# Performance work log

Measured on AMD Instinct MI355X. Metric: run time of the kernel, lower is better.

## Reference

```python
import math
import jax, jax.numpy as jnp
import numpy as np

B, L, C, H = 8, 1024, 1024, 16
D = C // H  # head_dim = 64
MAX_SCALE_MUL = math.log(100.0)


def setup_inputs() -> dict:
    key = jax.random.key(0)
    ks = jax.random.split(key, 8)
    x = jax.random.normal(ks[0], (B, L, C), dtype=jnp.float32)
    # rotary frequencies: angle(l, j) = l * theta^(-2j/D), stored as (cos, sin)
    theta = 10000.0
    inv_freq = theta ** (-jnp.arange(0, D, 2, dtype=jnp.float32) / D)  # [D/2]
    ang = jnp.arange(L, dtype=jnp.float32)[:, None] * inv_freq[None, :]  # [L, D/2]
    freqs_cis = jnp.stack([jnp.cos(ang), jnp.sin(ang)], axis=-1)  # [L, D/2, 2]
    attn_bias = jnp.zeros((1, 1, L, L), dtype=jnp.float32)
    W_qkv = jax.random.normal(ks[1], (3 * C, C), dtype=jnp.float32) * (1.0 / math.sqrt(C))
    q_bias = jnp.zeros((C,), dtype=jnp.float32)
    v_bias = jnp.zeros((C,), dtype=jnp.float32)
    scale_mul_log = jnp.full((1, H, 1, 1), math.log(4.0), dtype=jnp.float32)
    W_proj = jax.random.normal(ks[2], (C, C), dtype=jnp.float32) * (1.0 / math.sqrt(C))
    b_proj = jnp.zeros((C,), dtype=jnp.float32)
    return {"x": x, "freqs_cis": freqs_cis, "attn_bias": attn_bias,
            "W_qkv": W_qkv, "q_bias": q_bias, "v_bias": v_bias,
            "scale_mul_log": scale_mul_log, "W_proj": W_proj, "b_proj": b_proj}


def _l2norm(t):
    # F.normalize(t, dim=-1): t / max(||t||_2, eps)
    n = jnp.sqrt(jnp.sum(t * t, axis=-1, keepdims=True))
    return t / jnp.maximum(n, 1e-12)


def _rope(t, fr):
    # t: [B,H,L,D]; fr: [L,D/2,2] (cos,sin). Complex mul on adjacent pairs.
    b, h, l, d = t.shape
    t2 = t.reshape(b, h, l, d // 2, 2)
    c = fr[None, None, :, :, 0]
    s = fr[None, None, :, :, 1]
    re = t2[..., 0] * c - t2[..., 1] * s
    im = t2[..., 0] * s + t2[..., 1] * c
    return jnp.stack([re, im], axis=-1).reshape(b, h, l, d)


def reference(x, freqs_cis, attn_bias, W_qkv, q_bias, v_bias, scale_mul_log, W_proj, b_proj):
    b, l, c = x.shape
    bias = jnp.concatenate([q_bias, jnp.zeros_like(q_bias), v_bias])  # [3C]
    qkv = (x @ W_qkv.T + bias).reshape(b, l, 3, H, D)
    # permute(2,0,3,1,4) -> q,k,v each [B,H,L,D]
    q = jnp.transpose(qkv[:, :, 0], (0, 2, 1, 3))
    k = jnp.transpose(qkv[:, :, 1], (0, 2, 1, 3))
    v = jnp.transpose(qkv[:, :, 2], (0, 2, 1, 3))
    # attn_l2_norm path: learned per-head scale, softmax scale = 1
    scale_mul = jnp.exp(jnp.minimum(scale_mul_log, MAX_SCALE_MUL))  # [1,H,1,1]
    q = _l2norm(q) * scale_mul
    k = _l2norm(k)
    q = _rope(q, freqs_cis)
    k = _rope(k, freqs_cis)
    scores = jnp.einsum('bhqd,bhkd->bhqk', q, k) * 1.0 + attn_bias
    attn = jax.nn.softmax(scores, axis=-1)
    out = jnp.einsum('bhqk,bhkd->bhqd', attn, v)
    out = jnp.transpose(out, (0, 2, 1, 3)).reshape(b, l, c)
    return out @ W_proj.T + b_proj
```

## Files before the change

### kernel.cpp

```cpp
#include <hip/hip_runtime.h>
#include <math.h>

#define PB 8
#define PL 1024
#define PC 1024
#define PH 16
#define PD 64
#define MAX_SCALE_MUL 4.605170185988092f
#define LOG2E 1.4426950408889634f

typedef __attribute__((ext_vector_type(8))) short s16x8;
typedef __attribute__((ext_vector_type(4))) float f32x4;

#define MFMA16(a, b, c) __builtin_amdgcn_mfma_f32_16x16x32_bf16(a, b, c, 0, 0, 0)

#if __has_builtin(__builtin_amdgcn_exp2f)
#define EXP2(x) __builtin_amdgcn_exp2f(x)
#else
#define EXP2(x) exp2f(x)
#endif

__device__ __forceinline__ unsigned short f2bf(float f) {
    unsigned u = __float_as_uint(f);
    unsigned r = (u + 0x7fffu + ((u >> 16) & 1u)) >> 16;
    return (unsigned short)r;
}

__device__ __forceinline__ unsigned pk2bf(float a, float b) {
#if __has_builtin(__builtin_amdgcn_cvt_pk_bf16_f32)
    typedef __attribute__((ext_vector_type(2))) __bf16 bf16x2_t;
    bf16x2_t r = __builtin_amdgcn_cvt_pk_bf16_f32(a, b);
    return __builtin_bit_cast(unsigned, r);
#else
    return (unsigned)f2bf(a) | ((unsigned)f2bf(b) << 16);
#endif
}

__device__ __forceinline__ void gl2lds16(const void* g, void* l) {
    __builtin_amdgcn_global_load_lds(
        (const __attribute__((address_space(1))) unsigned int*)g,
        (__attribute__((address_space(3))) unsigned int*)l, 16, 0, 0);
}

__global__ __launch_bounds__(256) void bias_flag_kernel(
    const float* __restrict__ bias, int* __restrict__ flag)
{
    int idx = blockIdx.x * 256 + threadIdx.x;
    const float4* b4 = (const float4*)bias;
    bool nz = false;
#pragma unroll
    for (int i = 0; i < 4; i++) {
        float4 v = b4[idx * 4 + i];
        nz |= (v.x != 0.f) | (v.y != 0.f) | (v.z != 0.f) | (v.w != 0.f);
    }
    if (nz) atomicOr(flag, 1);
}

__global__ __launch_bounds__(256) void cast3_kernel(
    const float* __restrict__ a, const float* __restrict__ b,
    const float* __restrict__ c,
    unsigned short* __restrict__ oa, unsigned short* __restrict__ ob,
    unsigned short* __restrict__ oc)
{
    int blk = blockIdx.x;
    const float* src; unsigned short* dst; int base;
    if (blk < 8192)       { src = a; dst = oa; base = blk; }
    else if (blk < 11264) { src = b; dst = ob; base = blk - 8192; }
    else                  { src = c; dst = oc; base = blk - 11264; }
    int i = base * 256 + threadIdx.x;
    float4 v = ((const float4*)src)[i];
    ((uint2*)dst)[i] = make_uint2(pk2bf(v.x, v.y), pk2bf(v.z, v.w));
}

__global__ __launch_bounds__(256) void gemm_qkv_lean(
    const unsigned short* __restrict__ Xh,
    const unsigned short* __restrict__ Wh,
    const float* __restrict__ qb, const float* __restrict__ vb,
    unsigned short* __restrict__ Qh, unsigned short* __restrict__ Kh,
    unsigned short* __restrict__ Vh)
{
    __shared__ unsigned short As[128 * 32];
    __shared__ unsigned short Bs[128 * 32];
    const int tid  = threadIdx.x;
    const int wave = tid >> 6, lane = tid & 63;
    const int wm = wave & 1, wn = wave >> 1;
    const int quad = lane >> 4, rr = lane & 15;
    const int m0 = blockIdx.x * 128, n0 = blockIdx.y * 128;

    f32x4 acc[4][4];
#pragma unroll
    for (int i = 0; i < 4; i++)
#pragma unroll
        for (int j = 0; j < 4; j++) acc[i][j] = (f32x4){0.f, 0.f, 0.f, 0.f};

    const int rw = lane >> 2;
    const int cc = lane & 3;
    const int g  = cc ^ ((rw >> 1) & 3);
    const int srow = wave * 32 + rw;
    const unsigned short* gA0 = Xh + (size_t)(m0 + srow) * 1024 + g * 8;
    const unsigned short* gA1 = gA0 + (size_t)16 * 1024;
    const unsigned short* gB0 = Wh + (size_t)(n0 + srow) * 1024 + g * 8;
    const unsigned short* gB1 = gB0 + (size_t)16 * 1024;
    unsigned short* lA0 = &As[(wave * 32) * 32];
    unsigned short* lA1 = &As[(wave * 32 + 16) * 32];
    unsigned short* lB0 = &Bs[(wave * 32) * 32];
    unsigned short* lB1 = &Bs[(wave * 32 + 16) * 32];

    const int swz = (rr >> 1) & 3;
    const int coff = ((quad ^ swz) * 8);

    for (int k0 = 0; k0 < 1024; k0 += 32) {
        gl2lds16(gA0, lA0); gl2lds16(gA1, lA1);
        gl2lds16(gB0, lB0); gl2lds16(gB1, lB1);
        gA0 += 32; gA1 += 32; gB0 += 32; gB1 += 32;
        __syncthreads();

        s16x8 af[4], bf[4];
#pragma unroll
        for (int i = 0; i < 4; i++)
            af[i] = *(const s16x8*)&As[(wm * 64 + i * 16 + rr) * 32 + coff];
#pragma unroll
        for (int j = 0; j < 4; j++)
            bf[j] = *(const s16x8*)&Bs[(wn * 64 + j * 16 + rr) * 32 + coff];
#pragma unroll
        for (int i = 0; i < 4; i++)
#pragma unroll
            for (int j = 0; j < 4; j++)
                acc[i][j] = MFMA16(af[i], bf[j], acc[i][j]);
        __syncthreads();
    }

    const int b     = m0 >> 10;
    const int which = n0 >> 10;
    const int h     = ((n0 & 1023) + wn * 64) >> 6;
    const int lb0   = (m0 & 1023) + wm * 64;
    unsigned short* dst = (which == 0) ? Qh : ((which == 1) ? Kh : Vh);
    unsigned short* base = dst + ((size_t)(b * PH + h) * PL) * PD;

#pragma unroll
    for (int j = 0; j < 4; j++) {
        const int d = j * 16 + rr;
        float bias = 0.f;
        if (which == 0) bias = qb[h * 64 + d];
        if (which == 2) bias = vb[h * 64 + d];
#pragma unroll
        for (int i = 0; i < 4; i++) {
            const int l = lb0 + i * 16 + quad * 4;
#pragma unroll
            for (int reg = 0; reg < 4; reg++)
                base[(size_t)(l + reg) * PD + d] = f2bf(acc[i][j][reg] + bias);
        }
    }
}

__global__ __launch_bounds__(256) void postproc_kernel(
    unsigned short* __restrict__ Qh, unsigned short* __restrict__ Kh,
    const unsigned short* __restrict__ Vh, unsigned short* __restrict__ Vt,
    const float* __restrict__ freqs, const float* __restrict__ sml)
{
    const int blk = blockIdx.x;
    const int tid = threadIdx.x;

    if (blk < 32768) {
        const bool isQ = blk < 16384;
        const int rb = isQ ? blk : blk - 16384;
        const int row = rb * 8 + (tid >> 5);
        const int li  = tid & 31;
        const int h = (row >> 10) & (PH - 1);
        const int l = row & (PL - 1);

        unsigned short* buf = isQ ? Qh : Kh;
        unsigned* p = (unsigned*)(buf + (size_t)row * PD) + li;
        unsigned v = *p;
        float v0 = __uint_as_float(v << 16);
        float v1 = __uint_as_float(v & 0xffff0000u);

        float ss = fmaf(v0, v0, v1 * v1);
#pragma unroll
        for (int off = 1; off <= 16; off <<= 1) ss += __shfl_xor(ss, off);

        float smul = isQ ? (__expf(fminf(sml[h], MAX_SCALE_MUL)) * LOG2E) : 1.0f;
        float scale = smul / fmaxf(sqrtf(ss), 1e-12f);
        v0 *= scale; v1 *= scale;

        float2 cs = ((const float2*)freqs)[l * 32 + li];
        float re = v0 * cs.x - v1 * cs.y;
        float im = fmaf(v0, cs.y, v1 * cs.x);
        *p = pk2bf(re, im);
        return;
    }

    const int vblk = blk - 32768;
    const int bh = vblk >> 4;
    const int l0 = (vblk & 15) * 64;
#pragma unroll
    for (int s = 0; s < 2; s++) {
        int slot = s * 256 + tid;
        int d  = slot & 63;
        int lb = l0 + (slot >> 6) * 8;
        unsigned o[4];
#pragma unroll
        for (int i = 0; i < 4; i++) {
            unsigned short a0 = Vh[((size_t)bh * PL + lb + 2 * i) * PD + d];
            unsigned short a1 = Vh[((size_t)bh * PL + lb + 2 * i + 1) * PD + d];
            o[i] = (unsigned)a0 | ((unsigned)a1 << 16);
        }
        *(uint4*)&Vt[((size_t)bh * PD + d) * PL + lb] = make_uint4(o[0], o[1], o[2], o[3]);
    }
}

__global__ __launch_bounds__(256) void attn_mfma(
    const unsigned short* __restrict__ Qh, const unsigned short* __restrict__ Kh,
    const unsigned short* __restrict__ Vt, const float* __restrict__ bias,
    const float* __restrict__ sml, const int* __restrict__ biasflag,
    unsigned short* __restrict__ O)
{
    __shared__ unsigned short Ks[64 * 64];
    __shared__ unsigned short Vs[64 * 64];
    __shared__ unsigned int   Ps[4][16 * 36];

    const int tid  = threadIdx.x;
    const int wave = tid >> 6, lane = tid & 63;
    const int quad = lane >> 4, rr = lane & 15;
    const int bh = blockIdx.x, q0 = blockIdx.y * 128;
    const int b = bh >> 4, h = bh & 15;
    const int hasbias = *biasflag;

    const float M = __expf(fminf(sml[h], MAX_SCALE_MUL)) * LOG2E;
    const f32x4 negM = (f32x4){-M, -M, -M, -M};

    const int sr = wave * 16 + (lane >> 3);
    const int sc = lane & 7;
    const int sg = sc ^ (sr & 7);
    const int swz8 = rr & 7;

    const size_t kvbase = (size_t)bh * PL * PD;

    s16x8 qB[2][2];
#pragma unroll
    for (int g = 0; g < 2; g++) {
        const size_t qrow = (size_t)bh * PL + q0 + g * 64 + wave * 16 + rr;
        qB[g][0] = *(const s16x8*)(Qh + qrow * PD + quad * 8);
        qB[g][1] = *(const s16x8*)(Qh + qrow * PD + 32 + quad * 8);
    }

    f32x4 accO[2][4];
#pragma unroll
    for (int g = 0; g < 2; g++)
#pragma unroll
        for (int jd = 0; jd < 4; jd++) accO[g][jd] = (f32x4){0.f, 0.f, 0.f, 0.f};
    float lsum[2] = {0.f, 0.f};

    for (int kb = 0; kb < 16; kb++) {
        gl2lds16(Kh + kvbase + (size_t)(kb * 64 + sr) * PD + sg * 8, &Ks[(wave * 16) * 64]);
        gl2lds16(Kh + kvbase + (size_t)(kb * 64 + sr + 8) * PD + sg * 8, &Ks[(wave * 16 + 8) * 64]);
        gl2lds16(Vt + kvbase + (size_t)sr * PL + kb * 64 + sg * 8, &Vs[(wave * 16) * 64]);
        gl2lds16(Vt + kvbase + (size_t)(sr + 8) * PL + kb * 64 + sg * 8, &Vs[(wave * 16 + 8) * 64]);
        __syncthreads();

        s16x8 kA[4][2];
#pragma unroll
        for (int s = 0; s < 4; s++) {
            kA[s][0] = *(const s16x8*)&Ks[(s * 16 + rr) * 64 + ((0 + quad) ^ swz8) * 8];
            kA[s][1] = *(const s16x8*)&Ks[(s * 16 + rr) * 64 + ((4 + quad) ^ swz8) * 8];
        }
        f32x4 sc4[2][4];
#pragma unroll
        for (int g = 0; g < 2; g++)
#pragma unroll
            for (int s = 0; s < 4; s++) {
                f32x4 z = MFMA16(kA[s][0], qB[g][0], negM);
                z = MFMA16(kA[s][1], qB[g][1], z);
                sc4[g][s] = z;
            }

        if (hasbias) {
#pragma unroll
            for (int g = 0; g < 2; g++) {
                const float* brow = bias + (size_t)(q0 + g * 64 + wave * 16 + rr) * PL + kb * 64;
#pragma unroll
                for (int s = 0; s < 4; s++) {
                    float4 bv = *(const float4*)(brow + s * 16 + quad * 4);
                    sc4[g][s][0] = fmaf(bv.x, LOG2E, sc4[g][s][0]);
                    sc4[g][s][1] = fmaf(bv.y, LOG2E, sc4[g][s][1]);
                    sc4[g][s][2] = fmaf(bv.z, LOG2E, sc4[g][s][2]);
                    sc4[g][s][3] = fmaf(bv.w, LOG2E, sc4[g][s][3]);
                }
            }
        }

#pragma unroll
        for (int g = 0; g < 2; g++)
#pragma unroll
            for (int s = 0; s < 4; s++) {
                sc4[g][s][0] = EXP2(sc4[g][s][0]);
                sc4[g][s][1] = EXP2(sc4[g][s][1]);
                sc4[g][s][2] = EXP2(sc4[g][s][2]);
                sc4[g][s][3] = EXP2(sc4[g][s][3]);
                lsum[g] += sc4[g][s][0] + sc4[g][s][1] + sc4[g][s][2] + sc4[g][s][3];
            }

        s16x8 vA[4][2];
#pragma unroll
        for (int s = 0; s < 4; s++) {
            vA[s][0] = *(const s16x8*)&Vs[(s * 16 + rr) * 64 + ((0 + quad) ^ swz8) * 8];
            vA[s][1] = *(const s16x8*)&Vs[(s * 16 + rr) * 64 + ((4 + quad) ^ swz8) * 8];
        }
#pragma unroll
        for (int g = 0; g < 2; g++) {
#pragma unroll
            for (int s = 0; s < 4; s++) {
                *(uint2*)&Ps[wave][rr * 36 + s * 8 + quad * 2] =
                    make_uint2(pk2bf(sc4[g][s][0], sc4[g][s][1]),
                               pk2bf(sc4[g][s][2], sc4[g][s][3]));
            }
            s16x8 pB0 = *(const s16x8*)&Ps[wave][rr * 36 + quad * 4];
            s16x8 pB1 = *(const s16x8*)&Ps[wave][rr * 36 + 16 + quad * 4];
#pragma unroll
            for (int jd = 0; jd < 4; jd++) {
                accO[g][jd] = MFMA16(vA[jd][0], pB0, accO[g][jd]);
                accO[g][jd] = MFMA16(vA[jd][1], pB1, accO[g][jd]);
            }
        }
        __syncthreads();
    }

    const int lr = lane >> 2, cch = lane & 3;
#pragma unroll
    for (int g = 0; g < 2; g++) {
        float ls = lsum[g];
        ls += __shfl_xor(ls, 16);
        ls += __shfl_xor(ls, 32);
        float inv = 1.0f / ls;
#pragma unroll
        for (int jd = 0; jd < 4; jd++) {
            *(uint2*)&Ps[wave][rr * 36 + jd * 8 + quad * 2] =
                make_uint2(pk2bf(accO[g][jd][0] * inv, accO[g][jd][1] * inv),
                           pk2bf(accO[g][jd][2] * inv, accO[g][jd][3] * inv));
        }
        uint4 w0 = *(const uint4*)&Ps[wave][lr * 36 + cch * 8];
        uint4 w1 = *(const uint4*)&Ps[wave][lr * 36 + cch * 8 + 4];
        size_t ob = ((size_t)(b * PL + q0 + g * 64 + wave * 16 + lr) * PC + h * PD);
        *(uint4*)(O + ob + cch * 16)     = w0;
        *(uint4*)(O + ob + cch * 16 + 8) = w1;
    }
}

__global__ __launch_bounds__(256) void gemm_proj_mfma(
    const unsigned short* __restrict__ Ah,
    const unsigned short* __restrict__ Wh,
    const float* __restrict__ bp, float* __restrict__ Out)
{
    __shared__ unsigned short As[128 * 32];
    __shared__ unsigned short Bs[128 * 32];
    const int tid  = threadIdx.x;
    const int wave = tid >> 6, lane = tid & 63;
    const int wm = wave & 1, wn = wave >> 1;
    const int quad = lane >> 4, rr = lane & 15;
    const int m0 = blockIdx.x * 128, n0 = blockIdx.y * 128;

    f32x4 acc[4][4];
#pragma unroll
    for (int i = 0; i < 4; i++)
#pragma unroll
        for (int j = 0; j < 4; j++) acc[i][j] = (f32x4){0.f, 0.f, 0.f, 0.f};

    const int rw = lane >> 2;
    const int cc = lane & 3;
    const int g  = cc ^ ((rw >> 1) & 3);
    const int srow = wave * 32 + rw;
    const unsigned short* gA0 = Ah + (size_t)(m0 + srow) * 1024 + g * 8;
    const unsigned short* gA1 = gA0 + (size_t)16 * 1024;
    const unsigned short* gB0 = Wh + (size_t)(n0 + srow) * 1024 + g * 8;
    const unsigned short* gB1 = gB0 + (size_t)16 * 1024;
    unsigned short* lA0 = &As[(wave * 32) * 32];
    unsigned short* lA1 = &As[(wave * 32 + 16) * 32];
    unsigned short* lB0 = &Bs[(wave * 32) * 32];
    unsigned short* lB1 = &Bs[(wave * 32 + 16) * 32];

    const int swz = (rr >> 1) & 3;
    const int coff = ((quad ^ swz) * 8);

    for (int k0 = 0; k0 < 1024; k0 += 32) {
        gl2lds16(gA0, lA0); gl2lds16(gA1, lA1);
        gl2lds16(gB0, lB0); gl2lds16(gB1, lB1);
        gA0 += 32; gA1 += 32; gB0 += 32; gB1 += 32;
        __syncthreads();

        s16x8 af[4], bf[4];
#pragma unroll
        for (int i = 0; i < 4; i++)
            af[i] = *(const s16x8*)&As[(wm * 64 + i * 16 + rr) * 32 + coff];
#pragma unroll
        for (int j = 0; j < 4; j++)
            bf[j] = *(const s16x8*)&Bs[(wn * 64 + j * 16 + rr) * 32 + coff];
#pragma unroll
        for (int i = 0; i < 4; i++)
#pragma unroll
            for (int j = 0; j < 4; j++)
                acc[i][j] = MFMA16(af[i], bf[j], acc[i][j]);
        __syncthreads();
    }

#pragma unroll
    for (int i = 0; i < 4; i++) {
        const int mb = m0 + wm * 64 + i * 16 + quad * 4;
#pragma unroll
        for (int j = 0; j < 4; j++) {
            const int n = n0 + wn * 64 + j * 16 + rr;
            const float bb = bp[n];
#pragma unroll
            for (int reg = 0; reg < 4; reg++)
                Out[(size_t)(mb + reg) * 1024 + n] = acc[i][j][reg] + bb;
        }
    }
}

extern "C" void kernel_launch(void* const* d_in, const int* in_sizes, int n_in,
                              void* d_out, int out_size, void* d_ws, size_t ws_size,
                              hipStream_t stream)
{
    const float* x         = (const float*)d_in[0];
    const float* freqs     = (const float*)d_in[1];
    const float* attn_bias = (const float*)d_in[2];
    const float* W_qkv     = (const float*)d_in[3];
    const float* q_bias    = (const float*)d_in[4];
    const float* v_bias    = (const float*)d_in[5];
    const float* sml       = (const float*)d_in[6];
    const float* W_proj    = (const float*)d_in[7];
    const float* b_proj    = (const float*)d_in[8];
    float* out = (float*)d_out;

    unsigned char* w = (unsigned char*)d_ws;
    const size_t MB = 1ull << 20;
    unsigned short* xh  = (unsigned short*)(w + 0);
    unsigned short* wqh = (unsigned short*)(w + 16 * MB);
    unsigned short* wph = (unsigned short*)(w + 22 * MB);
    unsigned short* Qh  = (unsigned short*)(w + 24 * MB);
    unsigned short* Kh  = (unsigned short*)(w + 40 * MB);
    unsigned short* Vh  = (unsigned short*)(w + 56 * MB);
    unsigned short* Vt  = (unsigned short*)(w + 72 * MB);
    unsigned short* Oh  = (unsigned short*)(w + 88 * MB);
    int*            flg = (int*)(w + 104 * MB);

    hipMemsetAsync(flg, 0, sizeof(int), stream);
    bias_flag_kernel<<<256, 256, 0, stream>>>(attn_bias, flg);
    cast3_kernel<<<12288, 256, 0, stream>>>(x, W_qkv, W_proj, xh, wqh, wph);
    gemm_qkv_lean<<<dim3(64, 24), 256, 0, stream>>>(xh, wqh, q_bias, v_bias, Qh, Kh, Vh);
    postproc_kernel<<<34816, 256, 0, stream>>>(Qh, Kh, Vh, Vt, freqs, sml);
    attn_mfma<<<dim3(128, 8), 256, 0, stream>>>(Qh, Kh, Vt, attn_bias, sml, flg, Oh);
    gemm_proj_mfma<<<dim3(64, 8), 256, 0, stream>>>(Oh, wph, b_proj, out);
}
```

Measured before the change: 288.7 us.

## Load K/V directly from global in attention and vectorize QKV epilogue stores

The attention kernel drops LDS staging of K and V tiles and block-wide barriers, having each wave read its MFMA fragments straight from global memory/L2. Each block now covers 64 queries instead of 128, so twice as many blocks are launched. The QKV GEMM swaps its operand roles so the accumulator layout puts four consecutive head-dim values per lane, allowing packed 8-byte stores and a vectorized bias load. The trade is more redundant global/L2 traffic for K/V, since four waves each reread the same tiles, in exchange for no syncs and higher occupancy.

```diff
diff --git a/kernel.cpp b/kernel.cpp
--- a/kernel.cpp
+++ b/kernel.cpp
@@ -115,18 +115,18 @@
         gA0 += 32; gA1 += 32; gB0 += 32; gB1 += 32;
         __syncthreads();
 
-        s16x8 af[4], bf[4];
+        s16x8 wf[4], xf[4];
 #pragma unroll
         for (int i = 0; i < 4; i++)
-            af[i] = *(const s16x8*)&As[(wm * 64 + i * 16 + rr) * 32 + coff];
+            wf[i] = *(const s16x8*)&Bs[(wn * 64 + i * 16 + rr) * 32 + coff];
 #pragma unroll
         for (int j = 0; j < 4; j++)
-            bf[j] = *(const s16x8*)&Bs[(wn * 64 + j * 16 + rr) * 32 + coff];
+            xf[j] = *(const s16x8*)&As[(wm * 64 + j * 16 + rr) * 32 + coff];
 #pragma unroll
         for (int i = 0; i < 4; i++)
 #pragma unroll
             for (int j = 0; j < 4; j++)
-                acc[i][j] = MFMA16(af[i], bf[j], acc[i][j]);
+                acc[i][j] = MFMA16(wf[i], xf[j], acc[i][j]);
         __syncthreads();
     }
 
@@ -136,19 +136,20 @@
     const int lb0   = (m0 & 1023) + wm * 64;
     unsigned short* dst = (which == 0) ? Qh : ((which == 1) ? Kh : Vh);
     unsigned short* base = dst + ((size_t)(b * PH + h) * PL) * PD;
-
-#pragma unroll
-    for (int j = 0; j < 4; j++) {
-        const int d = j * 16 + rr;
-        float bias = 0.f;
-        if (which == 0) bias = qb[h * 64 + d];
-        if (which == 2) bias = vb[h * 64 + d];
-#pragma unroll
-        for (int i = 0; i < 4; i++) {
-            const int l = lb0 + i * 16 + quad * 4;
-#pragma unroll
-            for (int reg = 0; reg < 4; reg++)
-                base[(size_t)(l + reg) * PD + d] = f2bf(acc[i][j][reg] + bias);
+    const float* bvec = (which == 0) ? qb : vb;
+
+#pragma unroll
+    for (int i = 0; i < 4; i++) {
+        const int d0 = i * 16 + quad * 4;
+        float4 b4 = make_float4(0.f, 0.f, 0.f, 0.f);
+        if (which != 1) b4 = *(const float4*)(bvec + h * 64 + d0);
+#pragma unroll
+        for (int j = 0; j < 4; j++) {
+            const int l = lb0 + j * 16 + rr;
+            uint2 pk = make_uint2(
+                pk2bf(acc[i][j][0] + b4.x, acc[i][j][1] + b4.y),
+                pk2bf(acc[i][j][2] + b4.z, acc[i][j][3] + b4.w));
+            *(uint2*)(base + (size_t)l * PD + d0) = pk;
         }
     }
 }
@@ -215,135 +216,109 @@
     const float* __restrict__ sml, const int* __restrict__ biasflag,
     unsigned short* __restrict__ O)
 {
-    __shared__ unsigned short Ks[64 * 64];
-    __shared__ unsigned short Vs[64 * 64];
-    __shared__ unsigned int   Ps[4][16 * 36];
+    __shared__ unsigned int Ps[4][16 * 36];
 
     const int tid  = threadIdx.x;
     const int wave = tid >> 6, lane = tid & 63;
     const int quad = lane >> 4, rr = lane & 15;
-    const int bh = blockIdx.x, q0 = blockIdx.y * 128;
+    const int bh = blockIdx.x, q0 = blockIdx.y * 64;
     const int b = bh >> 4, h = bh & 15;
     const int hasbias = *biasflag;
 
     const float M = __expf(fminf(sml[h], MAX_SCALE_MUL)) * LOG2E;
     const f32x4 negM = (f32x4){-M, -M, -M, -M};
 
-    const int sr = wave * 16 + (lane >> 3);
-    const int sc = lane & 7;
-    const int sg = sc ^ (sr & 7);
-    const int swz8 = rr & 7;
-
-    const size_t kvbase = (size_t)bh * PL * PD;
-
-    s16x8 qB[2][2];
-#pragma unroll
-    for (int g = 0; g < 2; g++) {
-        const size_t qrow = (size_t)bh * PL + q0 + g * 64 + wave * 16 + rr;
-        qB[g][0] = *(const s16x8*)(Qh + qrow * PD + quad * 8);
-        qB[g][1] = *(const s16x8*)(Qh + qrow * PD + 32 + quad * 8);
-    }
-
-    f32x4 accO[2][4];
-#pragma unroll
-    for (int g = 0; g < 2; g++)
-#pragma unroll
-        for (int jd = 0; jd < 4; jd++) accO[g][jd] = (f32x4){0.f, 0.f, 0.f, 0.f};
-    float lsum[2] = {0.f, 0.f};
-
+    const unsigned short* Kb = Kh + (size_t)bh * PL * PD;
+    const unsigned short* Vb = Vt + (size_t)bh * PL * PD;
+
+    const size_t qrow = (size_t)bh * PL + q0 + wave * 16 + rr;
+    const s16x8 qB0 = *(const s16x8*)(Qh + qrow * PD + quad * 8);
+    const s16x8 qB1 = *(const s16x8*)(Qh + qrow * PD + 32 + quad * 8);
+
+    f32x4 accO[4];
+#pragma unroll
+    for (int jd = 0; jd < 4; jd++) accO[jd] = (f32x4){0.f, 0.f, 0.f, 0.f};
+    float lsum = 0.f;
+
+    const int qglob = q0 + wave * 16 + rr;
+
+#pragma unroll 1
     for (int kb = 0; kb < 16; kb++) {
-        gl2lds16(Kh + kvbase + (size_t)(kb * 64 + sr) * PD + sg * 8, &Ks[(wave * 16) * 64]);
-        gl2lds16(Kh + kvbase + (size_t)(kb * 64 + sr + 8) * PD + sg * 8, &Ks[(wave * 16 + 8) * 64]);
-        gl2lds16(Vt + kvbase + (size_t)sr * PL + kb * 64 + sg * 8, &Vs[(wave * 16) * 64]);
-        gl2lds16(Vt + kvbase + (size_t)(sr + 8) * PL + kb * 64 + sg * 8, &Vs[(wave * 16 + 8) * 64]);
-        __syncthreads();
-
         s16x8 kA[4][2];
 #pragma unroll
         for (int s = 0; s < 4; s++) {
-            kA[s][0] = *(const s16x8*)&Ks[(s * 16 + rr) * 64 + ((0 + quad) ^ swz8) * 8];
-            kA[s][1] = *(const s16x8*)&Ks[(s * 16 + rr) * 64 + ((4 + quad) ^ swz8) * 8];
-        }
-        f32x4 sc4[2][4];
-#pragma unroll
-        for (int g = 0; g < 2; g++)
+            const unsigned short* kp = Kb + (size_t)(kb * 64 + s * 16 + rr) * PD;
+            kA[s][0] = *(const s16x8*)(kp + quad * 8);
+            kA[s][1] = *(const s16x8*)(kp + 32 + quad * 8);
+        }
+        f32x4 sc4[4];
+#pragma unroll
+        for (int s = 0; s < 4; s++) {
+            f32x4 z = MFMA16(kA[s][0], qB0, negM);
+            z = MFMA16(kA[s][1], qB1, z);
+            sc4[s] = z;
+        }
+
+        if (hasbias) {
+            const float* brow = bias + (size_t)qglob * PL + kb * 64;
 #pragma unroll
             for (int s = 0; s < 4; s++) {
-                f32x4 z = MFMA16(kA[s][0], qB[g][0], negM);
-                z = MFMA16(kA[s][1], qB[g][1], z);
-                sc4[g][s] = z;
+                float4 bv = *(const float4*)(brow + s * 16 + quad * 4);
+                sc4[s][0] = fmaf(bv.x, LOG2E, sc4[s][0]);
+                sc4[s][1] = fmaf(bv.y, LOG2E, sc4[s][1]);
+                sc4[s][2] = fmaf(bv.z, LOG2E, sc4[s][2]);
+                sc4[s][3] = fmaf(bv.w, LOG2E, sc4[s][3]);
             }
-
-        if (hasbias) {
-#pragma unroll
-            for (int g = 0; g < 2; g++) {
-                const float* brow = bias + (size_t)(q0 + g * 64 + wave * 16 + rr) * PL + kb * 64;
-#pragma unroll
-                for (int s = 0; s < 4; s++) {
-                    float4 bv = *(const float4*)(brow + s * 16 + quad * 4);
-                    sc4[g][s][0] = fmaf(bv.x, LOG2E, sc4[g][s][0]);
-                    sc4[g][s][1] = fmaf(bv.y, LOG2E, sc4[g][s][1]);
-                    sc4[g][s][2] = fmaf(bv.z, LOG2E, sc4[g][s][2]);
-                    sc4[g][s][3] = fmaf(bv.w, LOG2E, sc4[g][s][3]);
-                }
-            }
-        }
-
-#pragma unroll
-        for (int g = 0; g < 2; g++)
-#pragma unroll
-            for (int s = 0; s < 4; s++) {
-                sc4[g][s][0] = EXP2(sc4[g][s][0]);
-                sc4[g][s][1] = EXP2(sc4[g][s][1]);
-                sc4[g][s][2] = EXP2(sc4[g][s][2]);
-                sc4[g][s][3] = EXP2(sc4[g][s][3]);
-                lsum[g] += sc4[g][s][0] + sc4[g][s][1] + sc4[g][s][2] + sc4[g][s][3];
-            }
+        }
+
+#pragma unroll
+        for (int s = 0; s < 4; s++) {
+            sc4[s][0] = EXP2(sc4[s][0]);
+            sc4[s][1] = EXP2(sc4[s][1]);
+            sc4[s][2] = EXP2(sc4[s][2]);
+            sc4[s][3] = EXP2(sc4[s][3]);
+            lsum += sc4[s][0] + sc4[s][1] + sc4[s][2] + sc4[s][3];
+        }
 
         s16x8 vA[4][2];
 #pragma unroll
         for (int s = 0; s < 4; s++) {
-            vA[s][0] = *(const s16x8*)&Vs[(s * 16 + rr) * 64 + ((0 + quad) ^ swz8) * 8];
-            vA[s][1] = *(const s16x8*)&Vs[(s * 16 + rr) * 64 + ((4 + quad) ^ swz8) * 8];
-        }
-#pragma unroll
-        for (int g = 0; g < 2; g++) {
-#pragma unroll
-            for (int s = 0; s < 4; s++) {
-                *(uint2*)&Ps[wave][rr * 36 + s * 8 + quad * 2] =
-                    make_uint2(pk2bf(sc4[g][s][0], sc4[g][s][1]),
-                               pk2bf(sc4[g][s][2], sc4[g][s][3]));
-            }
-            s16x8 pB0 = *(const s16x8*)&Ps[wave][rr * 36 + quad * 4];
-            s16x8 pB1 = *(const s16x8*)&Ps[wave][rr * 36 + 16 + quad * 4];
-#pragma unroll
-            for (int jd = 0; jd < 4; jd++) {
-                accO[g][jd] = MFMA16(vA[jd][0], pB0, accO[g][jd]);
-                accO[g][jd] = MFMA16(vA[jd][1], pB1, accO[g][jd]);
-            }
-        }
-        __syncthreads();
-    }
-
+            const unsigned short* vp = Vb + (size_t)(s * 16 + rr) * PL + kb * 64;
+            vA[s][0] = *(const s16x8*)(vp + quad * 8);
+            vA[s][1] = *(const s16x8*)(vp + 32 + quad * 8);
+        }
+
+#pragma unroll
+        for (int s = 0; s < 4; s++) {
+            *(uint2*)&Ps[wave][rr * 36 + s * 8 + quad * 2] =
+                make_uint2(pk2bf(sc4[s][0], sc4[s][1]),
+                           pk2bf(sc4[s][2], sc4[s][3]));
+        }
+        s16x8 pB0 = *(const s16x8*)&Ps[wave][rr * 36 + quad * 4];
+        s16x8 pB1 = *(const s16x8*)&Ps[wave][rr * 36 + 16 + quad * 4];
+
+#pragma unroll
+        for (int jd = 0; jd < 4; jd++) {
+            accO[jd] = MFMA16(vA[jd][0], pB0, accO[jd]);
+            accO[jd] = MFMA16(vA[jd][1], pB1, accO[jd]);
+        }
+    }
+
+    lsum += __shfl_xor(lsum, 16);
+    lsum += __shfl_xor(lsum, 32);
+    float inv = 1.0f / lsum;
+#pragma unroll
+    for (int jd = 0; jd < 4; jd++) {
+        *(uint2*)&Ps[wave][rr * 36 + jd * 8 + quad * 2] =
+            make_uint2(pk2bf(accO[jd][0] * inv, accO[jd][1] * inv),
+                       pk2bf(accO[jd][2] * inv, accO[jd][3] * inv));
+    }
     const int lr = lane >> 2, cch = lane & 3;
-#pragma unroll
-    for (int g = 0; g < 2; g++) {
-        float ls = lsum[g];
-        ls += __shfl_xor(ls, 16);
-        ls += __shfl_xor(ls, 32);
-        float inv = 1.0f / ls;
-#pragma unroll
-        for (int jd = 0; jd < 4; jd++) {
-            *(uint2*)&Ps[wave][rr * 36 + jd * 8 + quad * 2] =
-                make_uint2(pk2bf(accO[g][jd][0] * inv, accO[g][jd][1] * inv),
-                           pk2bf(accO[g][jd][2] * inv, accO[g][jd][3] * inv));
-        }
-        uint4 w0 = *(const uint4*)&Ps[wave][lr * 36 + cch * 8];
-        uint4 w1 = *(const uint4*)&Ps[wave][lr * 36 + cch * 8 + 4];
-        size_t ob = ((size_t)(b * PL + q0 + g * 64 + wave * 16 + lr) * PC + h * PD);
-        *(uint4*)(O + ob + cch * 16)     = w0;
-        *(uint4*)(O + ob + cch * 16 + 8) = w1;
-    }
+    uint4 w0 = *(const uint4*)&Ps[wave][lr * 36 + cch * 8];
+    uint4 w1 = *(const uint4*)&Ps[wave][lr * 36 + cch * 8 + 4];
+    size_t ob = ((size_t)(b * PL + q0 + wave * 16 + lr) * PC + h * PD);
+    *(uint4*)(O + ob + cch * 16)     = w0;
+    *(uint4*)(O + ob + cch * 16 + 8) = w1;
 }
 
 __global__ __launch_bounds__(256) void gemm_proj_mfma(
@@ -448,6 +423,6 @@
     cast3_kernel<<<12288, 256, 0, stream>>>(x, W_qkv, W_proj, xh, wqh, wph);
     gemm_qkv_lean<<<dim3(64, 24), 256, 0, stream>>>(xh, wqh, q_bias, v_bias, Qh, Kh, Vh);
     postproc_kernel<<<34816, 256, 0, stream>>>(Qh, Kh, Vh, Vt, freqs, sml);
-    attn_mfma<<<dim3(128, 8), 256, 0, stream>>>(Qh, Kh, Vt, attn_bias, sml, flg, Oh);
+    attn_mfma<<<dim3(128, 16), 256, 0, stream>>>(Qh, Kh, Vt, attn_bias, sml, flg, Oh);
     gemm_proj_mfma<<<dim3(64, 8), 256, 0, stream>>>(Oh, wph, b_proj, out);
 }
```

New measurement: 455.4 us. 1.58x slower.
